# Optimization experiments

Hardware: AMD Instinct MI355X
Metric: run time of the kernel (lower is better)

The kernel has to match this reference:

```python
import jax, jax.numpy as jnp
import numpy as np


def setup_inputs() -> dict:
    key = jax.random.key(0)
    B, L, C = 64, 2048, 1024  # sequences, per-seq length, n_classes
    T = B * L                 # total ragged tokens
    k1, k2 = jax.random.split(key)
    outputs = jax.random.normal(k1, (T, C), dtype=jnp.float32)
    targets = jax.random.randint(k2, (T,), 0, C)
    lengths = jnp.full((B,), L, dtype=jnp.int32)  # sum(lengths) == T
    return {"outputs": outputs, "targets": targets, "lengths": lengths, "gamma": 2.0}


def reference(outputs, targets, lengths, gamma):
    T = outputs.shape[0]
    B = lengths.shape[0]
    # per-token cross-entropy, reduction='none'
    logp = jax.nn.log_softmax(outputs, axis=-1)
    loss = -jnp.take_along_axis(logp, targets[:, None], axis=1)[:, 0]  # [T]
    # ragged segment structure
    seg = jnp.repeat(jnp.arange(B), lengths, total_repeat_length=T)  # segment id per token
    starts = jnp.cumsum(lengths) - lengths                           # segment offsets
    pos = jnp.arange(T) - starts[seg]                                # position within segment
    Ls = lengths[seg]
    # linspace(-gamma, gamma, L)[pos]; L==1 -> -gamma (matches torch.linspace)
    denom = jnp.maximum(Ls - 1, 1).astype(loss.dtype)
    raw = -gamma + (2.0 * gamma) * pos.astype(loss.dtype) / denom
    # per-segment softmax; per-segment max of raw is <= gamma, subtract for stability
    e = jnp.exp(raw - gamma)
    ssum = jax.ops.segment_sum(e, seg, num_segments=B)
    w = e / ssum[seg]
    return jnp.dot(loss, w) / B
```

## Files before the change

### kernel.cpp

```cpp
#include <hip/hip_runtime.h>
#include <math.h>

#define MAXB 1024
#define NBLK 2048

__global__ void esl_setup(const int* __restrict__ lengths, int B,
                          const float* __restrict__ gamma_p,
                          int* __restrict__ starts,
                          float* __restrict__ inv_ssum) {
    const int tid = threadIdx.x;
    if (tid == 0) {
        int acc = 0;
        starts[0] = 0;
        for (int b = 0; b < B; ++b) { acc += lengths[b]; starts[b + 1] = acc; }
    }
    const float g = gamma_p[0];
    for (int b = tid; b < B; b += blockDim.x) {
        const int L = lengths[b];
        if (L <= 0) { inv_ssum[b] = 0.f; continue; }
        const int dni = (L - 1) > 1 ? (L - 1) : 1;
        const float a = 2.f * g / (float)dni;
        float ss;
        if (fabsf(a) < 1e-20f) ss = (float)L * __expf(-2.f * g);
        else ss = __expf(-2.f * g) * (expm1f(a * (float)L) / expm1f(a));
        inv_ssum[b] = 1.f / ss;
    }
}

__global__ __launch_bounds__(256)
void esl_main(const float* __restrict__ outputs,
              const int* __restrict__ targets,
              const int* __restrict__ lengths,
              const int* __restrict__ g_starts,
              const float* __restrict__ g_inv,
              const float* __restrict__ gamma_p,
              int T, int B, int C, int inblock,
              float* __restrict__ partials) {
    __shared__ int   sh_starts[MAXB + 1];
    __shared__ float sh_inv[MAXB];
    __shared__ float sh_part[4];

    const int tid = threadIdx.x;
    const float g = gamma_p[0];

    if (inblock) {
        if (tid < 64) {
            const int b = tid;
            const int len = (b < B) ? lengths[b] : 0;
            int sc = len;
            #pragma unroll
            for (int off = 1; off < 64; off <<= 1) {
                const int u = __shfl_up(sc, off, 64);
                if (tid >= off) sc += u;
            }
            if (b < B) {
                sh_starts[b] = sc - len;
                if (b == B - 1) sh_starts[B] = sc;
                float inv = 0.f;
                const int L = len;
                if (L > 0) {
                    const int dni = (L - 1) > 1 ? (L - 1) : 1;
                    const float a = 2.f * g / (float)dni;
                    float ss;
                    if (fabsf(a) < 1e-20f) ss = (float)L * __expf(-2.f * g);
                    else ss = __expf(-2.f * g) * (expm1f(a * (float)L) / expm1f(a));
                    inv = 1.f / ss;
                }
                sh_inv[b] = inv;
            }
        }
    } else {
        const int nb = (B < MAXB) ? B : MAXB;
        for (int i = tid; i < nb + 1; i += blockDim.x) sh_starts[i] = g_starts[i];
        for (int i = tid; i < nb;     i += blockDim.x) sh_inv[i]   = g_inv[i];
    }
    __syncthreads();

    const int wid  = tid >> 6;
    const int lane = tid & 63;
    const int stride = gridDim.x * 4;
    const int t0 = blockIdx.x * 4 + wid;
    const int* stp    = (B <= MAXB) ? sh_starts : g_starts;
    const float* invp = (B <= MAXB) ? sh_inv    : g_inv;

    float acc = 0.f;

    if (C == 1024) {
        float4 a0, a1, a2, a3;
        float xt = 0.f;
        if (t0 < T) {
            const float* rowp = outputs + (size_t)t0 * 1024;
            const float4* row = (const float4*)rowp;
            a0 = row[lane]; a1 = row[lane + 64]; a2 = row[lane + 128]; a3 = row[lane + 192];
            xt = rowp[targets[t0]];
        }
        for (int t = t0; t < T; t += stride) {
            const int tn = t + stride;
            const int tl = (tn < T) ? tn : t;
            const float* rowpn = outputs + (size_t)tl * 1024;
            const float4* rown = (const float4*)rowpn;
            const float4 b0 = rown[lane];
            const float4 b1 = rown[lane + 64];
            const float4 b2 = rown[lane + 128];
            const float4 b3 = rown[lane + 192];
            const float xtn = rowpn[targets[tl]];

            float s = __expf(a0.x) + __expf(a0.y) + __expf(a0.z) + __expf(a0.w)
                    + __expf(a1.x) + __expf(a1.y) + __expf(a1.z) + __expf(a1.w)
                    + __expf(a2.x) + __expf(a2.y) + __expf(a2.z) + __expf(a2.w)
                    + __expf(a3.x) + __expf(a3.y) + __expf(a3.z) + __expf(a3.w);
            #pragma unroll
            for (int off = 32; off; off >>= 1) s += __shfl_xor(s, off, 64);
            const float lse = __logf(s);

            int lo = 0, hi = B - 1;
            while (lo < hi) {
                const int mid = (lo + hi + 1) >> 1;
                if (stp[mid] <= t) lo = mid; else hi = mid - 1;
            }
            const int st  = stp[lo];
            const int L   = stp[lo + 1] - st;
            const int pos = t - st;
            const float dn  = (float)((L - 1) > 1 ? (L - 1) : 1);
            const float raw = -g + (2.f * g) * ((float)pos / dn);
            acc += (lse - xt) * __expf(raw - g) * invp[lo];

            a0 = b0; a1 = b1; a2 = b2; a3 = b3; xt = xtn;
        }
    } else {
        for (int t = t0; t < T; t += stride) {
            const float* rowp = outputs + (size_t)t * (size_t)C;
            const float xt = rowp[targets[t]];
            float m = -3.402823e38f, s = 0.f;
            for (int j = lane; j < C; j += 64) m = fmaxf(m, rowp[j]);
            #pragma unroll
            for (int off = 32; off; off >>= 1) m = fmaxf(m, __shfl_xor(m, off, 64));
            for (int j = lane; j < C; j += 64) s += __expf(rowp[j] - m);
            #pragma unroll
            for (int off = 32; off; off >>= 1) s += __shfl_xor(s, off, 64);
            const float lse = m + __logf(s);
            int lo = 0, hi = B - 1;
            while (lo < hi) {
                const int mid = (lo + hi + 1) >> 1;
                if (stp[mid] <= t) lo = mid; else hi = mid - 1;
            }
            const int st  = stp[lo];
            const int L   = stp[lo + 1] - st;
            const int pos = t - st;
            const float dn  = (float)((L - 1) > 1 ? (L - 1) : 1);
            const float raw = -g + (2.f * g) * ((float)pos / dn);
            acc += (lse - xt) * __expf(raw - g) * invp[lo];
        }
    }

    if (lane == 0) sh_part[wid] = acc;
    __syncthreads();
    if (tid == 0)
        partials[blockIdx.x] = sh_part[0] + sh_part[1] + sh_part[2] + sh_part[3];
}

__global__ __launch_bounds__(256)
void esl_finish(const float* __restrict__ partials, int n, int B,
                float* __restrict__ out) {
    __shared__ float sh[4];
    float s = 0.f;
    for (int i = threadIdx.x; i < n; i += blockDim.x) s += partials[i];
    #pragma unroll
    for (int off = 32; off; off >>= 1) s += __shfl_xor(s, off, 64);
    const int wid = threadIdx.x >> 6;
    if ((threadIdx.x & 63) == 0) sh[wid] = s;
    __syncthreads();
    if (threadIdx.x == 0) out[0] = (sh[0] + sh[1] + sh[2] + sh[3]) / (float)B;
}

extern "C" void kernel_launch(void* const* d_in, const int* in_sizes, int n_in,
                              void* d_out, int out_size, void* d_ws, size_t ws_size,
                              hipStream_t stream) {
    const float* outputs = (const float*)d_in[0];
    const int*   targets = (const int*)d_in[1];
    const int*   lengths = (const int*)d_in[2];
    const float* gamma   = (const float*)d_in[3];
    float* out = (float*)d_out;

    const int T = in_sizes[1];
    const int B = in_sizes[2];
    const int C = (int)(in_sizes[0] / T);

    int*   starts   = (int*)d_ws;
    float* inv_ssum = (float*)((char*)d_ws + sizeof(int) * (size_t)(B + 1));
    float* partials = inv_ssum + B;

    const int inblock = (B <= 64) ? 1 : 0;
    if (!inblock)
        esl_setup<<<1, 256, 0, stream>>>(lengths, B, gamma, starts, inv_ssum);

    int grid = NBLK;
    const int max_needed = (T + 3) / 4;
    if (grid > max_needed) grid = max_needed;
    esl_main<<<grid, 256, 0, stream>>>(outputs, targets, lengths, starts, inv_ssum,
                                       gamma, T, B, C, inblock, partials);
    esl_finish<<<1, 256, 0, stream>>>(partials, grid, B, out);
}
```

Before: 99.30 us.

## Give each wave a contiguous token range with incremental segment tracking

For the C==1024 path, each wave now processes a contiguous block of tokens instead of a grid-strided set. The binary search over segment starts runs once per wave, and the segment is then advanced incrementally with a precomputed slope and weight. Two rows are loaded and reduced together per iteration for more memory-level parallelism. This replaces the explicit register prefetch of the next row, and the contiguous per-wave ranges change the DRAM access pattern, which may hurt or help coalescing across waves.

```diff
diff --git a/kernel.cpp b/kernel.cpp
--- a/kernel.cpp
+++ b/kernel.cpp
@@ -25,6 +25,14 @@
         else ss = __expf(-2.f * g) * (expm1f(a * (float)L) / expm1f(a));
         inv_ssum[b] = 1.f / ss;
     }
+}
+
+__device__ __forceinline__ float sumexp16(const float4 v0, const float4 v1,
+                                          const float4 v2, const float4 v3) {
+    return __expf(v0.x) + __expf(v0.y) + __expf(v0.z) + __expf(v0.w)
+         + __expf(v1.x) + __expf(v1.y) + __expf(v1.z) + __expf(v1.w)
+         + __expf(v2.x) + __expf(v2.y) + __expf(v2.z) + __expf(v2.w)
+         + __expf(v3.x) + __expf(v3.y) + __expf(v3.z) + __expf(v3.w);
 }
 
 __global__ __launch_bounds__(256)
@@ -78,57 +86,92 @@
 
     const int wid  = tid >> 6;
     const int lane = tid & 63;
-    const int stride = gridDim.x * 4;
-    const int t0 = blockIdx.x * 4 + wid;
     const int* stp    = (B <= MAXB) ? sh_starts : g_starts;
     const float* invp = (B <= MAXB) ? sh_inv    : g_inv;
 
     float acc = 0.f;
 
     if (C == 1024) {
-        float4 a0, a1, a2, a3;
-        float xt = 0.f;
-        if (t0 < T) {
-            const float* rowp = outputs + (size_t)t0 * 1024;
-            const float4* row = (const float4*)rowp;
-            a0 = row[lane]; a1 = row[lane + 64]; a2 = row[lane + 128]; a3 = row[lane + 192];
-            xt = rowp[targets[t0]];
-        }
-        for (int t = t0; t < T; t += stride) {
-            const int tn = t + stride;
-            const int tl = (tn < T) ? tn : t;
-            const float* rowpn = outputs + (size_t)tl * 1024;
-            const float4* rown = (const float4*)rowpn;
-            const float4 b0 = rown[lane];
-            const float4 b1 = rown[lane + 64];
-            const float4 b2 = rown[lane + 128];
-            const float4 b3 = rown[lane + 192];
-            const float xtn = rowpn[targets[tl]];
-
-            float s = __expf(a0.x) + __expf(a0.y) + __expf(a0.z) + __expf(a0.w)
-                    + __expf(a1.x) + __expf(a1.y) + __expf(a1.z) + __expf(a1.w)
-                    + __expf(a2.x) + __expf(a2.y) + __expf(a2.z) + __expf(a2.w)
-                    + __expf(a3.x) + __expf(a3.y) + __expf(a3.z) + __expf(a3.w);
-            #pragma unroll
-            for (int off = 32; off; off >>= 1) s += __shfl_xor(s, off, 64);
-            const float lse = __logf(s);
-
+        const int nwaves = gridDim.x * 4;
+        const int w = blockIdx.x * 4 + wid;
+        const int npw = (T + nwaves - 1) / nwaves;
+        const int tbeg = w * npw;
+        const int tend = (tbeg + npw < T) ? tbeg + npw : T;
+
+        if (tbeg < T) {
             int lo = 0, hi = B - 1;
             while (lo < hi) {
                 const int mid = (lo + hi + 1) >> 1;
-                if (stp[mid] <= t) lo = mid; else hi = mid - 1;
-            }
-            const int st  = stp[lo];
-            const int L   = stp[lo + 1] - st;
-            const int pos = t - st;
-            const float dn  = (float)((L - 1) > 1 ? (L - 1) : 1);
-            const float raw = -g + (2.f * g) * ((float)pos / dn);
-            acc += (lse - xt) * __expf(raw - g) * invp[lo];
-
-            a0 = b0; a1 = b1; a2 = b2; a3 = b3; xt = xtn;
+                if (stp[mid] <= tbeg) lo = mid; else hi = mid - 1;
+            }
+            int seg = lo;
+            int st  = stp[seg];
+            int en  = stp[seg + 1];
+            float slope = 0.f, winv = 0.f;
+            {
+                const float dnl = fmaxf((float)(en - st) - 1.f, 1.f);
+                slope = __fdividef(2.f * g, dnl);
+                winv  = invp[seg];
+            }
+            const float n2g = -2.f * g;
+
+            #define ESL_ADV(tt)                                                    \
+                while ((tt) >= en) {                                               \
+                    ++seg; st = en; en = stp[seg + 1];                             \
+                    const float dnl_ = fmaxf((float)(en - st) - 1.f, 1.f);         \
+                    slope = __fdividef(2.f * g, dnl_);                             \
+                    winv  = invp[seg];                                             \
+                }
+
+            int t = tbeg;
+            for (; t + 1 < tend; t += 2) {
+                const float* rowA = outputs + (size_t)t * 1024;
+                const float* rowB = rowA + 1024;
+                const float4* ra = (const float4*)rowA;
+                const float4* rb = (const float4*)rowB;
+                const float4 a0 = ra[lane], a1 = ra[lane + 64],
+                             a2 = ra[lane + 128], a3 = ra[lane + 192];
+                const float4 b0 = rb[lane], b1 = rb[lane + 64],
+                             b2 = rb[lane + 128], b3 = rb[lane + 192];
+                const float xa = rowA[targets[t]];
+                const float xb = rowB[targets[t + 1]];
+
+                float sa = sumexp16(a0, a1, a2, a3);
+                float sb = sumexp16(b0, b1, b2, b3);
+                #pragma unroll
+                for (int off = 32; off; off >>= 1) {
+                    sa += __shfl_xor(sa, off, 64);
+                    sb += __shfl_xor(sb, off, 64);
+                }
+                const float lseA = __logf(sa);
+                const float lseB = __logf(sb);
+
+                ESL_ADV(t);
+                const float wA = __expf(fmaf((float)(t - st), slope, n2g)) * winv;
+                ESL_ADV(t + 1);
+                const float wB = __expf(fmaf((float)(t + 1 - st), slope, n2g)) * winv;
+
+                acc += (lseA - xa) * wA + (lseB - xb) * wB;
+            }
+            if (t < tend) {
+                const float* rowA = outputs + (size_t)t * 1024;
+                const float4* ra = (const float4*)rowA;
+                const float4 a0 = ra[lane], a1 = ra[lane + 64],
+                             a2 = ra[lane + 128], a3 = ra[lane + 192];
+                const float xa = rowA[targets[t]];
+                float sa = sumexp16(a0, a1, a2, a3);
+                #pragma unroll
+                for (int off = 32; off; off >>= 1) sa += __shfl_xor(sa, off, 64);
+                const float lseA = __logf(sa);
+                ESL_ADV(t);
+                const float wA = __expf(fmaf((float)(t - st), slope, n2g)) * winv;
+                acc += (lseA - xa) * wA;
+            }
+            #undef ESL_ADV
         }
     } else {
-        for (int t = t0; t < T; t += stride) {
+        const int stride = gridDim.x * 4;
+        for (int t = blockIdx.x * 4 + wid; t < T; t += stride) {
             const float* rowp = outputs + (size_t)t * (size_t)C;
             const float xt = rowp[targets[t]];
             float m = -3.402823e38f, s = 0.f;
```

Result: slower. 103.4 us (+4.1%).

## Precompute per-token segment weights in a separate prep kernel

Applied to the files above, without the earlier changes.

Moves the per-token binary search over segment starts and the weight exponent out of the bandwidth-bound main loop into a new prep kernel that writes a weights array. The main kernel now streams one extra float per token and does a single fma instead of a search plus shared-memory setup. This adds a kernel launch and an extra T-float write and read, in exchange for less per-row scalar work and no shared-memory setup in the main kernel.

```diff
diff --git a/kernel.cpp b/kernel.cpp
--- a/kernel.cpp
+++ b/kernel.cpp
@@ -28,18 +28,14 @@
 }
 
 __global__ __launch_bounds__(256)
-void esl_main(const float* __restrict__ outputs,
-              const int* __restrict__ targets,
-              const int* __restrict__ lengths,
+void esl_prep(const int* __restrict__ lengths,
               const int* __restrict__ g_starts,
               const float* __restrict__ g_inv,
               const float* __restrict__ gamma_p,
-              int T, int B, int C, int inblock,
-              float* __restrict__ partials) {
+              int T, int B, int inblock,
+              float* __restrict__ weights) {
     __shared__ int   sh_starts[MAXB + 1];
     __shared__ float sh_inv[MAXB];
-    __shared__ float sh_part[4];
-
     const int tid = threadIdx.x;
     const float g = gamma_p[0];
 
@@ -76,23 +72,58 @@
     }
     __syncthreads();
 
+    const int* stp    = (B <= MAXB) ? sh_starts : g_starts;
+    const float* invp = (B <= MAXB) ? sh_inv    : g_inv;
+
+    const int t = blockIdx.x * blockDim.x + tid;
+    if (t < T) {
+        int lo = 0, hi = B - 1;
+        while (lo < hi) {
+            const int mid = (lo + hi + 1) >> 1;
+            if (stp[mid] <= t) lo = mid; else hi = mid - 1;
+        }
+        const int st  = stp[lo];
+        const int L   = stp[lo + 1] - st;
+        const float dn = fmaxf((float)L - 1.f, 1.f);
+        const float raw = fmaf((float)(t - st), __fdividef(2.f * g, dn), -2.f * g);
+        weights[t] = __expf(raw) * invp[lo];
+    }
+}
+
+__device__ __forceinline__ float sumexp16(const float4 v0, const float4 v1,
+                                          const float4 v2, const float4 v3) {
+    return __expf(v0.x) + __expf(v0.y) + __expf(v0.z) + __expf(v0.w)
+         + __expf(v1.x) + __expf(v1.y) + __expf(v1.z) + __expf(v1.w)
+         + __expf(v2.x) + __expf(v2.y) + __expf(v2.z) + __expf(v2.w)
+         + __expf(v3.x) + __expf(v3.y) + __expf(v3.z) + __expf(v3.w);
+}
+
+__global__ __launch_bounds__(256)
+void esl_main(const float* __restrict__ outputs,
+              const int* __restrict__ targets,
+              const float* __restrict__ weights,
+              int T, int C,
+              float* __restrict__ partials) {
+    __shared__ float sh_part[4];
+
+    const int tid  = threadIdx.x;
     const int wid  = tid >> 6;
     const int lane = tid & 63;
     const int stride = gridDim.x * 4;
     const int t0 = blockIdx.x * 4 + wid;
-    const int* stp    = (B <= MAXB) ? sh_starts : g_starts;
-    const float* invp = (B <= MAXB) ? sh_inv    : g_inv;
 
     float acc = 0.f;
 
     if (C == 1024) {
         float4 a0, a1, a2, a3;
-        float xt = 0.f;
+        float xt = 0.f, wt = 0.f;
         if (t0 < T) {
             const float* rowp = outputs + (size_t)t0 * 1024;
             const float4* row = (const float4*)rowp;
-            a0 = row[lane]; a1 = row[lane + 64]; a2 = row[lane + 128]; a3 = row[lane + 192];
+            a0 = row[lane]; a1 = row[lane + 64];
+            a2 = row[lane + 128]; a3 = row[lane + 192];
             xt = rowp[targets[t0]];
+            wt = weights[t0];
         }
         for (int t = t0; t < T; t += stride) {
             const int tn = t + stride;
@@ -104,28 +135,14 @@
             const float4 b2 = rown[lane + 128];
             const float4 b3 = rown[lane + 192];
             const float xtn = rowpn[targets[tl]];
-
-            float s = __expf(a0.x) + __expf(a0.y) + __expf(a0.z) + __expf(a0.w)
-                    + __expf(a1.x) + __expf(a1.y) + __expf(a1.z) + __expf(a1.w)
-                    + __expf(a2.x) + __expf(a2.y) + __expf(a2.z) + __expf(a2.w)
-                    + __expf(a3.x) + __expf(a3.y) + __expf(a3.z) + __expf(a3.w);
+            const float wtn = weights[tl];
+
+            float s = sumexp16(a0, a1, a2, a3);
             #pragma unroll
             for (int off = 32; off; off >>= 1) s += __shfl_xor(s, off, 64);
-            const float lse = __logf(s);
-
-            int lo = 0, hi = B - 1;
-            while (lo < hi) {
-                const int mid = (lo + hi + 1) >> 1;
-                if (stp[mid] <= t) lo = mid; else hi = mid - 1;
-            }
-            const int st  = stp[lo];
-            const int L   = stp[lo + 1] - st;
-            const int pos = t - st;
-            const float dn  = (float)((L - 1) > 1 ? (L - 1) : 1);
-            const float raw = -g + (2.f * g) * ((float)pos / dn);
-            acc += (lse - xt) * __expf(raw - g) * invp[lo];
-
-            a0 = b0; a1 = b1; a2 = b2; a3 = b3; xt = xtn;
+            acc = fmaf(__logf(s) - xt, wt, acc);
+
+            a0 = b0; a1 = b1; a2 = b2; a3 = b3; xt = xtn; wt = wtn;
         }
     } else {
         for (int t = t0; t < T; t += stride) {
@@ -138,18 +155,7 @@
             for (int j = lane; j < C; j += 64) s += __expf(rowp[j] - m);
             #pragma unroll
             for (int off = 32; off; off >>= 1) s += __shfl_xor(s, off, 64);
-            const float lse = m + __logf(s);
-            int lo = 0, hi = B - 1;
-            while (lo < hi) {
-                const int mid = (lo + hi + 1) >> 1;
-                if (stp[mid] <= t) lo = mid; else hi = mid - 1;
-            }
-            const int st  = stp[lo];
-            const int L   = stp[lo + 1] - st;
-            const int pos = t - st;
-            const float dn  = (float)((L - 1) > 1 ? (L - 1) : 1);
-            const float raw = -g + (2.f * g) * ((float)pos / dn);
-            acc += (lse - xt) * __expf(raw - g) * invp[lo];
+            acc = fmaf(m + __logf(s) - xt, weights[t], acc);
         }
     }
 
@@ -189,15 +195,18 @@
     int*   starts   = (int*)d_ws;
     float* inv_ssum = (float*)((char*)d_ws + sizeof(int) * (size_t)(B + 1));
     float* partials = inv_ssum + B;
+    float* weights  = partials + NBLK;
 
     const int inblock = (B <= 64) ? 1 : 0;
     if (!inblock)
         esl_setup<<<1, 256, 0, stream>>>(lengths, B, gamma, starts, inv_ssum);
 
+    esl_prep<<<(T + 255) / 256, 256, 0, stream>>>(lengths, starts, inv_ssum, gamma,
+                                                  T, B, inblock, weights);
+
     int grid = NBLK;
     const int max_needed = (T + 3) / 4;
     if (grid > max_needed) grid = max_needed;
-    esl_main<<<grid, 256, 0, stream>>>(outputs, targets, lengths, starts, inv_ssum,
-                                       gamma, T, B, C, inblock, partials);
+    esl_main<<<grid, 256, 0, stream>>>(outputs, targets, weights, T, C, partials);
     esl_finish<<<1, 256, 0, stream>>>(partials, grid, B, out);
 }
```

Result: slower. 105.1 us (+5.9%).
